# Optimization experiments

Hardware: AMD Instinct MI355X
Metric: run time of the kernel (lower is better)

Reference implementation:

```python
import jax, jax.numpy as jnp
import numpy as np

VOXEL_SIZE = 0.4
STRIDE = 2
NUM_BATCH = 4
PRE_MAXSIZE = 1024  # nms_premaxsize
NMS_THR = 0.1
NEG_INF = -1e9


def setup_inputs() -> dict:
    key = jax.random.key(0)
    ks = jax.random.split(key, 7)
    N, C = 200000, 256
    feat = jax.random.normal(ks[0], (N, C), dtype=jnp.float32)
    batch_idx = jax.random.randint(ks[1], (N,), 0, NUM_BATCH, dtype=jnp.int32)
    coor = jax.random.randint(ks[2], (N, 2), 0, 400, dtype=jnp.int32)
    W_cls = jax.random.normal(ks[3], (C, 2), dtype=jnp.float32) * 0.02
    b_cls = jnp.zeros((2,), dtype=jnp.float32)
    W_reg = jax.random.normal(ks[4], (C, 9), dtype=jnp.float32) * 0.02
    b_reg = jnp.zeros((9,), dtype=jnp.float32)
    return {"feat": feat, "batch_idx": batch_idx, "coor": coor,
            "W_cls": W_cls, "b_cls": b_cls, "W_reg": W_reg, "b_reg": b_reg}


def _bev_iou(bx):
    # bx: [K,7] (x,y,z,l,w,h,r); axis-aligned BEV IoU on (x,y,l,w)
    x, y, l, w = bx[:, 0], bx[:, 1], bx[:, 3], bx[:, 4]
    x1, x2 = x - l / 2, x + l / 2
    y1, y2 = y - w / 2, y + w / 2
    ix = jnp.maximum(jnp.minimum(x2[:, None], x2[None, :]) - jnp.maximum(x1[:, None], x1[None, :]), 0.0)
    iy = jnp.maximum(jnp.minimum(y2[:, None], y2[None, :]) - jnp.maximum(y1[:, None], y1[None, :]), 0.0)
    inter = ix * iy
    area = l * w
    union = area[:, None] + area[None, :] - inter
    return inter / jnp.maximum(union, 1e-6)


def _nms_keep(iou):
    # greedy NMS over score-descending rows; returns keep mask [K]
    K = iou.shape[0]
    idx = jnp.arange(K)

    def body(i, supp):
        keep_i = jnp.logical_not(supp[i])
        new = keep_i & (iou[i] > NMS_THR) & (idx > i)
        return supp | new

    supp = jax.lax.fori_loop(0, K, body, jnp.zeros((K,), dtype=bool))
    return jnp.logical_not(supp)


def reference(feat, batch_idx, coor, W_cls, b_cls, W_reg, b_reg):
    # ---- shared heads over all sparse voxels ----
    cls_logits = feat @ W_cls + b_cls            # [N, 1+1] (neg evidence, class)
    probs = jax.nn.softmax(cls_logits, axis=-1)
    cls_prob = probs[:, 1:]                      # [N, n_cls]
    conf = jnp.max(cls_prob, axis=-1)            # [N]
    label = jnp.argmax(cls_prob, axis=-1)        # [N]

    reg = feat @ W_reg + b_reg                   # [N, 9] -> ctr(3) dim(3) dir(2) scr(1)
    ctr, dim, drn, scr = reg[:, :3], reg[:, 3:6], reg[:, 6:8], reg[:, 8]
    scr = jax.nn.sigmoid(scr)                    # sigmoid_keys=['scr']

    # indices2metric: voxel indices -> metric centers
    centers = coor.astype(jnp.float32) * (VOXEL_SIZE * STRIDE)  # [N, 2]

    xy = centers + ctr[:, :2]
    z = ctr[:, 2]
    lwh = jnp.exp(jnp.clip(dim, -6.0, 6.0))
    angle = jnp.arctan2(drn[:, 0], drn[:, 1])
    boxes = jnp.concatenate([xy, z[:, None], lwh, angle[:, None]], axis=-1)  # [N, 7]
    score = conf * scr                           # [N]

    def per_sample(b):
        s = jnp.where(batch_idx == b, score, NEG_INF)
        vals, idx = jax.lax.top_k(s, PRE_MAXSIZE)          # score-sorted (desc)
        bx = boxes[idx]                                     # [K, 7]
        lb = label[idx]                                     # [K]
        valid = vals > NEG_INF / 2
        iou = _bev_iou(bx)
        keep = _nms_keep(iou) & valid
        out = jnp.concatenate([bx, vals[:, None]], axis=-1) * keep[:, None]  # [K, 8]
        return out, lb, keep

    out, lb, keep = jax.vmap(per_sample)(jnp.arange(NUM_BATCH))
    return out, lb, keep
```

## Files before the change

kernel.cpp:

```cpp
#include <hip/hip_runtime.h>
#include <math.h>

#define NBATCH 4
#define PRE 1024
#define CAND 4096
#define NHIST 65536

__device__ __forceinline__ unsigned long long allow_mask(int i, int l) {
    int base = l << 6;
    if (i < base) return ~0ull;
    int sh = i - base + 1;
    if (sh >= 64) return 0ull;
    return (~0ull) << sh;
}

__global__ void k0_weights(const float* __restrict__ Wcls, const float* __restrict__ bcls,
                           const float* __restrict__ Wreg, const float* __restrict__ breg,
                           double* __restrict__ Wd, double* __restrict__ biasd) {
    int j = blockIdx.x;
    int c = threadIdx.x;
    float w = (j < 2) ? Wcls[c * 2 + j] : Wreg[c * 9 + (j - 2)];
    Wd[j * 256 + c] = (double)w;
    if (c == 0) biasd[j] = (double)((j < 2) ? bcls[j] : breg[j - 2]);
}

__global__ __launch_bounds__(256) void k1_points(
    const float4* __restrict__ feat4, const int* __restrict__ batch_idx,
    const int* __restrict__ coor, const double* __restrict__ Wd,
    const double* __restrict__ biasd, float* __restrict__ pointData,
    unsigned long long* __restrict__ keys, unsigned int* __restrict__ hist, int N) {
    __shared__ float sfeat[256 * 33];
    int tid = threadIdx.x;
    int p0 = blockIdx.x * 256;

    double acc[11];
#pragma unroll
    for (int j = 0; j < 11; ++j) acc[j] = 0.0;

    for (int ch = 0; ch < 8; ++ch) {
        int c0 = ch * 32;
        __syncthreads();
#pragma unroll
        for (int it = 0; it < 8; ++it) {
            int u = it * 256 + tid;
            int p = u >> 3, q = u & 7;
            int gp = p0 + p;
            float4 v = make_float4(0.f, 0.f, 0.f, 0.f);
            if (gp < N) v = feat4[gp * 64 + (c0 >> 2) + q];
            int base = p * 33 + q * 4;
            sfeat[base + 0] = v.x; sfeat[base + 1] = v.y;
            sfeat[base + 2] = v.z; sfeat[base + 3] = v.w;
        }
        __syncthreads();
        const double* wb = Wd + c0;
#pragma unroll 4
        for (int k = 0; k < 32; ++k) {
            double fv = (double)sfeat[tid * 33 + k];
#pragma unroll
            for (int j = 0; j < 11; ++j) acc[j] = fma(fv, wb[j * 256 + k], acc[j]);
        }
    }

    int p = p0 + tid;
    if (p >= N) return;

    double l0 = acc[0] + biasd[0], l1 = acc[1] + biasd[1];
    double conf = 1.0 / (1.0 + exp(-(l1 - l0)));
    double scr  = 1.0 / (1.0 + exp(-(acc[10] + biasd[10])));
    double score = conf * scr;
    float s32 = (float)score;

    double c0d = acc[2] + biasd[2], c1d = acc[3] + biasd[3], c2d = acc[4] + biasd[4];
    double d0 = acc[5] + biasd[5], d1 = acc[6] + biasd[6], d2 = acc[7] + biasd[7];
    double r0 = acc[8] + biasd[8], r1 = acc[9] + biasd[9];

    float cx = (float)coor[2 * p] * 0.8f;
    float cy = (float)coor[2 * p + 1] * 0.8f;
    float bx = (float)((double)cx + c0d);
    float by = (float)((double)cy + c1d);
    float bz = (float)c2d;
    float bl = (float)exp(fmin(fmax(d0, -6.0), 6.0));
    float bw = (float)exp(fmin(fmax(d1, -6.0), 6.0));
    float bh = (float)exp(fmin(fmax(d2, -6.0), 6.0));
    float ba = (float)atan2(r0, r1);

    float* pd = pointData + (size_t)p * 8;
    pd[0] = bx; pd[1] = by; pd[2] = bz; pd[3] = bl;
    pd[4] = bw; pd[5] = bh; pd[6] = ba; pd[7] = s32;
    keys[p] = (unsigned long long)__double_as_longlong(score);

    int b = batch_idx[p];
    unsigned int bucket = __float_as_uint(s32) >> 16;
    atomicAdd(&hist[b * NHIST + bucket], 1u);
}

__global__ __launch_bounds__(256) void k2_thresh(const unsigned int* __restrict__ hist,
                                                 unsigned int* __restrict__ Tarr) {
    int b = blockIdx.x, tid = threadIdx.x;
    __shared__ unsigned int csum[256];
    __shared__ unsigned int chunkv[256];
    __shared__ int stc;
    __shared__ unsigned int scum;
    const unsigned int* h = hist + b * NHIST;
    unsigned int s = 0;
    for (int m = 0; m < 256; ++m) s += h[tid * 256 + m];
    csum[tid] = s;
    __syncthreads();
    if (tid == 0) {
        unsigned int cum = 0; int tc = -1;
        for (int t = 255; t >= 0; --t) {
            if (cum + csum[t] >= 1024u) { tc = t; break; }
            cum += csum[t];
        }
        stc = tc; scum = cum;
    }
    __syncthreads();
    int tc = stc;
    if (tc < 0) { if (tid == 0) Tarr[b] = 0u; return; }
    chunkv[tid] = h[tc * 256 + tid];
    __syncthreads();
    if (tid == 0) {
        unsigned int cum = scum, T = (unsigned int)(tc * 256);
        for (int m = 255; m >= 0; --m) {
            unsigned int c = chunkv[m];
            if (cum + c >= 1024u) { T = (unsigned int)(tc * 256 + m); break; }
            cum += c;
        }
        Tarr[b] = T;
    }
}

__global__ void k3_compact(const int* __restrict__ batch_idx, const float* __restrict__ pointData,
                           const unsigned long long* __restrict__ keys,
                           const unsigned int* __restrict__ Tarr, unsigned int* __restrict__ candCount,
                           unsigned int* __restrict__ candIdx, unsigned long long* __restrict__ candKey,
                           int N) {
    int p = blockIdx.x * 256 + threadIdx.x;
    if (p >= N) return;
    int b = batch_idx[p];
    float s32 = pointData[(size_t)p * 8 + 7];
    unsigned int bucket = __float_as_uint(s32) >> 16;
    if (bucket >= Tarr[b]) {
        unsigned int pos = atomicAdd(&candCount[b], 1u);
        if (pos < CAND) {
            candIdx[b * CAND + pos] = (unsigned int)p;
            candKey[b * CAND + pos] = keys[p];
        }
    }
}

__global__ __launch_bounds__(1024) void k4_sort(const unsigned int* __restrict__ candCount,
                                                const unsigned int* __restrict__ candIdx,
                                                const unsigned long long* __restrict__ candKey,
                                                const float* __restrict__ pointData,
                                                float* __restrict__ topBox,
                                                unsigned int* __restrict__ validArr) {
    int b = blockIdx.x, tid = threadIdx.x;
    __shared__ unsigned long long ka[CAND];
    __shared__ unsigned int id[CAND];
    unsigned int cnt = candCount[b];
    if (cnt > CAND) cnt = CAND;
    for (int t = tid; t < CAND; t += 1024) {
        if ((unsigned int)t < cnt) {
            ka[t] = ~candKey[b * CAND + t];
            id[t] = candIdx[b * CAND + t];
        } else {
            ka[t] = ~0ull;
            id[t] = 0xFFFFFFFFu;
        }
    }
    __syncthreads();
    for (int k = 2; k <= CAND; k <<= 1) {
        for (int j = k >> 1; j > 0; j >>= 1) {
            for (int t = tid; t < CAND; t += 1024) {
                int l = t ^ j;
                if (l > t) {
                    bool up = ((t & k) == 0);
                    unsigned long long kt = ka[t], kl = ka[l];
                    unsigned int it_ = id[t], il = id[l];
                    bool gt = (kt > kl) || (kt == kl && it_ > il);
                    if (gt == up) { ka[t] = kl; ka[l] = kt; id[t] = il; id[l] = it_; }
                }
            }
            __syncthreads();
        }
    }
    unsigned int gi = id[tid];
    bool valid = (gi != 0xFFFFFFFFu) && ((unsigned int)tid < cnt);
    float v[8];
#pragma unroll
    for (int k = 0; k < 8; ++k) v[k] = 0.f;
    if (valid) {
        const float* pd = pointData + (size_t)gi * 8;
#pragma unroll
        for (int k = 0; k < 8; ++k) v[k] = pd[k];
    }
    float* tb = topBox + (size_t)(b * PRE + tid) * 8;
#pragma unroll
    for (int k = 0; k < 8; ++k) tb[k] = v[k];
    validArr[b * PRE + tid] = valid ? 1u : 0u;
}

__global__ __launch_bounds__(256) void k5_iou(const float* __restrict__ topBox,
                                              unsigned long long* __restrict__ M) {
    int wid = blockIdx.x * 4 + (threadIdx.x >> 6);
    int lane = threadIdx.x & 63;
    int b = wid >> 14;
    int rem = wid & 16383;
    int i = rem >> 4;
    int wj = rem & 15;
    const float* bi = topBox + (size_t)(b * PRE + i) * 8;
    int j = wj * 64 + lane;
    const float* bj = topBox + (size_t)(b * PRE + j) * 8;
    float xi = bi[0], yi = bi[1], li = bi[3], wi_ = bi[4];
    float xj = bj[0], yj = bj[1], lj = bj[3], wj_ = bj[4];
    float x1i = xi - li * 0.5f, x2i = xi + li * 0.5f;
    float y1i = yi - wi_ * 0.5f, y2i = yi + wi_ * 0.5f;
    float x1j = xj - lj * 0.5f, x2j = xj + lj * 0.5f;
    float y1j = yj - wj_ * 0.5f, y2j = yj + wj_ * 0.5f;
    float ix = fmaxf(fminf(x2i, x2j) - fmaxf(x1i, x1j), 0.0f);
    float iy = fmaxf(fminf(y2i, y2j) - fmaxf(y1i, y1j), 0.0f);
    float inter = ix * iy;
    float ai = li * wi_, aj = lj * wj_;
    float uni = ai + aj - inter;
    float iou = inter / fmaxf(uni, 1e-6f);
    unsigned long long m = __ballot(iou > 0.1f);
    if (lane == 0) M[(size_t)(b * PRE + i) * 16 + wj] = m;
}

__global__ __launch_bounds__(256) void k6_nms(const unsigned long long* __restrict__ M,
                                              const unsigned int* __restrict__ validArr,
                                              const float* __restrict__ topBox,
                                              float* __restrict__ out0,
                                              float* __restrict__ keepOut) {
    int b = blockIdx.x, tid = threadIdx.x;
    __shared__ unsigned int flag[PRE];
    __shared__ unsigned long long suppSh[16];
    for (int r = tid; r < PRE; r += 256) {
        const unsigned long long* row = M + (size_t)(b * PRE + r) * 16;
        unsigned long long o = 0ull;
#pragma unroll
        for (int l = 0; l < 16; ++l) o |= row[l] & allow_mask(r, l);
        flag[r] = (o != 0ull) ? 1u : 0u;
    }
    __syncthreads();
    if (tid < 64) {
        int lane = tid;
        unsigned long long supp = 0ull;
        for (int g = 0; g < 16; ++g) {
            unsigned long long act = __ballot(flag[g * 64 + lane] != 0u);
            while (act) {
                int bit = __builtin_ctzll(act);
                act &= act - 1ull;
                int i = g * 64 + bit;
                unsigned long long w = __shfl(supp, i >> 6);
                bool keep_i = ((w >> (i & 63)) & 1ull) == 0ull;
                if (keep_i && lane < 16) {
                    supp |= M[(size_t)(b * PRE + i) * 16 + lane] & allow_mask(i, lane);
                }
            }
        }
        if (lane < 16) suppSh[lane] = supp;
    }
    __syncthreads();
    for (int r = tid; r < PRE; r += 256) {
        bool keep = (((suppSh[r >> 6] >> (r & 63)) & 1ull) == 0ull) && (validArr[b * PRE + r] != 0u);
        float kf = keep ? 1.0f : 0.0f;
        const float* tb = topBox + (size_t)(b * PRE + r) * 8;
        float* o = out0 + (size_t)(b * PRE + r) * 8;
#pragma unroll
        for (int k = 0; k < 8; ++k) o[k] = tb[k] * kf;
        keepOut[b * PRE + r] = kf;
    }
}

extern "C" void kernel_launch(void* const* d_in, const int* in_sizes, int n_in,
                              void* d_out, int out_size, void* d_ws, size_t ws_size,
                              hipStream_t stream) {
    int N = in_sizes[0] / 256;
    const float* feat = (const float*)d_in[0];
    const int* batch_idx = (const int*)d_in[1];
    const int* coor = (const int*)d_in[2];
    const float* Wcls = (const float*)d_in[3];
    const float* bcls = (const float*)d_in[4];
    const float* Wreg = (const float*)d_in[5];
    const float* breg = (const float*)d_in[6];

    char* ws = (char*)d_ws;
    size_t off = 0;
    auto take = [&](size_t bytes) -> char* {
        char* r = ws + off;
        off += (bytes + 255) & ~(size_t)255;
        return r;
    };
    float* pointData = (float*)take((size_t)N * 8 * 4);
    unsigned long long* keys = (unsigned long long*)take((size_t)N * 8);
    unsigned int* hist = (unsigned int*)take((size_t)NBATCH * NHIST * 4);
    unsigned int* Tarr = (unsigned int*)take(NBATCH * 4);
    unsigned int* candCount = (unsigned int*)take(NBATCH * 4);
    unsigned int* candIdx = (unsigned int*)take(NBATCH * CAND * 4);
    unsigned long long* candKey = (unsigned long long*)take(NBATCH * CAND * 8);
    float* topBox = (float*)take(NBATCH * PRE * 8 * 4);
    unsigned int* validArr = (unsigned int*)take(NBATCH * PRE * 4);
    unsigned long long* M = (unsigned long long*)take((size_t)NBATCH * PRE * 16 * 8);
    double* Wd = (double*)take(11 * 256 * 8);
    double* biasd = (double*)take(11 * 8);

    float* out0 = (float*)d_out;
    float* keepOut = out0 + NBATCH * PRE * 8 + NBATCH * PRE;

    hipMemsetAsync(d_out, 0, (size_t)out_size * 4, stream);
    hipMemsetAsync(hist, 0, (size_t)NBATCH * NHIST * 4, stream);
    hipMemsetAsync(candCount, 0, NBATCH * 4, stream);

    int pb = (N + 255) / 256;
    k0_weights<<<dim3(11), dim3(256), 0, stream>>>(Wcls, bcls, Wreg, breg, Wd, biasd);
    k1_points<<<dim3(pb), dim3(256), 0, stream>>>((const float4*)feat, batch_idx, coor,
                                                  Wd, biasd, pointData, keys, hist, N);
    k2_thresh<<<dim3(NBATCH), dim3(256), 0, stream>>>(hist, Tarr);
    k3_compact<<<dim3(pb), dim3(256), 0, stream>>>(batch_idx, pointData, keys, Tarr,
                                                   candCount, candIdx, candKey, N);
    k4_sort<<<dim3(NBATCH), dim3(1024), 0, stream>>>(candCount, candIdx, candKey,
                                                     pointData, topBox, validArr);
    k5_iou<<<dim3(NBATCH * PRE * 16 / 4), dim3(256), 0, stream>>>(topBox, M);
    k6_nms<<<dim3(NBATCH), dim3(256), 0, stream>>>(M, validArr, topBox, out0, keepOut);
}
```

Before: 506.2 us.

## Split head GEMV into fp64 score and fp32 box paths, shrink sort and NMS work

The point kernel now keeps only the class logits and score channel in double precision and computes the eight box-regression channels in fp32. It splits each point's 256 channels across four threads and reduces the partial sums through shared memory. The bitonic sort uses 2048 elements when the candidate count allows it, IoU warps skip tiles below the diagonal, and NMS caches the nonzero suppression rows in LDS so the serial loop avoids global reads. The fp32 box path can change rounding relative to the double path, and the 64-point blocks add a shared-memory reduction step.

```diff
diff --git a/kernel.cpp b/kernel.cpp
--- a/kernel.cpp
+++ b/kernel.cpp
@@ -5,6 +5,7 @@
 #define PRE 1024
 #define CAND 4096
 #define NHIST 65536
+#define MAXSLOT 384
 
 __device__ __forceinline__ unsigned long long allow_mask(int i, int l) {
     int base = l << 6;
@@ -16,82 +17,114 @@
 
 __global__ void k0_weights(const float* __restrict__ Wcls, const float* __restrict__ bcls,
                            const float* __restrict__ Wreg, const float* __restrict__ breg,
-                           double* __restrict__ Wd, double* __restrict__ biasd) {
+                           double* __restrict__ Wd3, float* __restrict__ Wf8,
+                           double* __restrict__ biasD, float* __restrict__ biasF) {
     int j = blockIdx.x;
     int c = threadIdx.x;
-    float w = (j < 2) ? Wcls[c * 2 + j] : Wreg[c * 9 + (j - 2)];
-    Wd[j * 256 + c] = (double)w;
-    if (c == 0) biasd[j] = (double)((j < 2) ? bcls[j] : breg[j - 2]);
+    if (j < 2) {
+        Wd3[j * 256 + c] = (double)Wcls[c * 2 + j];
+        if (c == 0) biasD[j] = (double)bcls[j];
+    } else if (j == 10) {
+        Wd3[2 * 256 + c] = (double)Wreg[c * 9 + 8];
+        if (c == 0) biasD[2] = (double)breg[8];
+    } else {
+        int r = j - 2;
+        Wf8[r * 256 + c] = Wreg[c * 9 + r];
+        if (c == 0) biasF[r] = breg[r];
+    }
 }
 
 __global__ __launch_bounds__(256) void k1_points(
     const float4* __restrict__ feat4, const int* __restrict__ batch_idx,
-    const int* __restrict__ coor, const double* __restrict__ Wd,
-    const double* __restrict__ biasd, float* __restrict__ pointData,
+    const int* __restrict__ coor, const double* __restrict__ Wd3,
+    const float* __restrict__ Wf8, const double* __restrict__ biasD,
+    const float* __restrict__ biasF, float* __restrict__ pointData,
     unsigned long long* __restrict__ keys, unsigned int* __restrict__ hist, int N) {
-    __shared__ float sfeat[256 * 33];
+    __shared__ float4 smem4[64 * 68 / 4];
+    float* sfeat = (float*)smem4;
     int tid = threadIdx.x;
-    int p0 = blockIdx.x * 256;
-
-    double acc[11];
-#pragma unroll
-    for (int j = 0; j < 11; ++j) acc[j] = 0.0;
-
-    for (int ch = 0; ch < 8; ++ch) {
-        int c0 = ch * 32;
+    int q = tid >> 6;
+    int p = tid & 63;
+    int p0 = blockIdx.x * 64;
+
+    double accD0 = 0.0, accD1 = 0.0, accD2 = 0.0;
+    float accF[8];
+#pragma unroll
+    for (int j = 0; j < 8; ++j) accF[j] = 0.f;
+
+    for (int c = 0; c < 4; ++c) {
         __syncthreads();
 #pragma unroll
-        for (int it = 0; it < 8; ++it) {
+        for (int it = 0; it < 4; ++it) {
             int u = it * 256 + tid;
-            int p = u >> 3, q = u & 7;
-            int gp = p0 + p;
+            int pl = u >> 4, f4 = u & 15;
+            int gp = p0 + pl;
             float4 v = make_float4(0.f, 0.f, 0.f, 0.f);
-            if (gp < N) v = feat4[gp * 64 + (c0 >> 2) + q];
-            int base = p * 33 + q * 4;
-            sfeat[base + 0] = v.x; sfeat[base + 1] = v.y;
-            sfeat[base + 2] = v.z; sfeat[base + 3] = v.w;
+            if (gp < N) v = feat4[(size_t)gp * 64 + c * 16 + f4];
+            *(float4*)(sfeat + pl * 68 + f4 * 4) = v;
         }
         __syncthreads();
-        const double* wb = Wd + c0;
-#pragma unroll 4
-        for (int k = 0; k < 32; ++k) {
-            double fv = (double)sfeat[tid * 33 + k];
-#pragma unroll
-            for (int j = 0; j < 11; ++j) acc[j] = fma(fv, wb[j * 256 + k], acc[j]);
-        }
-    }
-
-    int p = p0 + tid;
-    if (p >= N) return;
-
-    double l0 = acc[0] + biasd[0], l1 = acc[1] + biasd[1];
-    double conf = 1.0 / (1.0 + exp(-(l1 - l0)));
-    double scr  = 1.0 / (1.0 + exp(-(acc[10] + biasd[10])));
-    double score = conf * scr;
-    float s32 = (float)score;
-
-    double c0d = acc[2] + biasd[2], c1d = acc[3] + biasd[3], c2d = acc[4] + biasd[4];
-    double d0 = acc[5] + biasd[5], d1 = acc[6] + biasd[6], d2 = acc[7] + biasd[7];
-    double r0 = acc[8] + biasd[8], r1 = acc[9] + biasd[9];
-
-    float cx = (float)coor[2 * p] * 0.8f;
-    float cy = (float)coor[2 * p + 1] * 0.8f;
-    float bx = (float)((double)cx + c0d);
-    float by = (float)((double)cy + c1d);
-    float bz = (float)c2d;
-    float bl = (float)exp(fmin(fmax(d0, -6.0), 6.0));
-    float bw = (float)exp(fmin(fmax(d1, -6.0), 6.0));
-    float bh = (float)exp(fmin(fmax(d2, -6.0), 6.0));
-    float ba = (float)atan2(r0, r1);
-
-    float* pd = pointData + (size_t)p * 8;
-    pd[0] = bx; pd[1] = by; pd[2] = bz; pd[3] = bl;
-    pd[4] = bw; pd[5] = bh; pd[6] = ba; pd[7] = s32;
-    keys[p] = (unsigned long long)__double_as_longlong(score);
-
-    int b = batch_idx[p];
-    unsigned int bucket = __float_as_uint(s32) >> 16;
-    atomicAdd(&hist[b * NHIST + bucket], 1u);
+        int chb = c * 64 + q * 16;
+        const double* w0 = Wd3 + chb;
+        const float* wf = Wf8 + chb;
+#pragma unroll
+        for (int k4 = 0; k4 < 4; ++k4) {
+            float4 v = *(const float4*)(sfeat + p * 68 + q * 16 + k4 * 4);
+            float vv[4] = {v.x, v.y, v.z, v.w};
+#pragma unroll
+            for (int m = 0; m < 4; ++m) {
+                int k = k4 * 4 + m;
+                double fd = (double)vv[m];
+                accD0 = fma(fd, w0[k], accD0);
+                accD1 = fma(fd, w0[256 + k], accD1);
+                accD2 = fma(fd, w0[512 + k], accD2);
+#pragma unroll
+                for (int j = 0; j < 8; ++j) accF[j] = fmaf(vv[m], wf[j * 256 + k], accF[j]);
+            }
+        }
+    }
+    __syncthreads();
+    double* pD = (double*)smem4;
+    float* pF = (float*)smem4 + 1536;
+    pD[tid * 3 + 0] = accD0; pD[tid * 3 + 1] = accD1; pD[tid * 3 + 2] = accD2;
+#pragma unroll
+    for (int j = 0; j < 8; ++j) pF[tid * 8 + j] = accF[j];
+    __syncthreads();
+    if (tid < 64) {
+        int gp = p0 + tid;
+        if (gp < N) {
+            double d0 = biasD[0], d1 = biasD[1], d2 = biasD[2];
+            float f[8];
+#pragma unroll
+            for (int j = 0; j < 8; ++j) f[j] = biasF[j];
+#pragma unroll
+            for (int qq = 0; qq < 4; ++qq) {
+                int base = qq * 64 + tid;
+                d0 += pD[base * 3 + 0]; d1 += pD[base * 3 + 1]; d2 += pD[base * 3 + 2];
+#pragma unroll
+                for (int j = 0; j < 8; ++j) f[j] += pF[base * 8 + j];
+            }
+            double conf = 1.0 / (1.0 + exp(-(d1 - d0)));
+            double scr = 1.0 / (1.0 + exp(-d2));
+            double score = conf * scr;
+            float s32 = (float)score;
+
+            float cx = (float)coor[2 * gp] * 0.8f;
+            float cy = (float)coor[2 * gp + 1] * 0.8f;
+            float bx = cx + f[0], by = cy + f[1], bz = f[2];
+            float bl = expf(fminf(fmaxf(f[3], -6.f), 6.f));
+            float bw = expf(fminf(fmaxf(f[4], -6.f), 6.f));
+            float bh = expf(fminf(fmaxf(f[5], -6.f), 6.f));
+            float ba = atan2f(f[6], f[7]);
+
+            float4* pd = (float4*)(pointData + (size_t)gp * 8);
+            pd[0] = make_float4(bx, by, bz, bl);
+            pd[1] = make_float4(bw, bh, ba, s32);
+            keys[gp] = (unsigned long long)__double_as_longlong(score);
+            int b = batch_idx[gp];
+            atomicAdd(&hist[b * NHIST + (__float_as_uint(s32) >> 16)], 1u);
+        }
+    }
 }
 
 __global__ __launch_bounds__(256) void k2_thresh(const unsigned int* __restrict__ hist,
@@ -160,7 +193,8 @@
     __shared__ unsigned int id[CAND];
     unsigned int cnt = candCount[b];
     if (cnt > CAND) cnt = CAND;
-    for (int t = tid; t < CAND; t += 1024) {
+    int n = (cnt <= 2048u) ? 2048 : 4096;
+    for (int t = tid; t < n; t += 1024) {
         if ((unsigned int)t < cnt) {
             ka[t] = ~candKey[b * CAND + t];
             id[t] = candIdx[b * CAND + t];
@@ -170,9 +204,9 @@
         }
     }
     __syncthreads();
-    for (int k = 2; k <= CAND; k <<= 1) {
+    for (int k = 2; k <= n; k <<= 1) {
         for (int j = k >> 1; j > 0; j >>= 1) {
-            for (int t = tid; t < CAND; t += 1024) {
+            for (int t = tid; t < n; t += 1024) {
                 int l = t ^ j;
                 if (l > t) {
                     bool up = ((t & k) == 0);
@@ -209,6 +243,7 @@
     int rem = wid & 16383;
     int i = rem >> 4;
     int wj = rem & 15;
+    if (wj < (i >> 6)) return;
     const float* bi = topBox + (size_t)(b * PRE + i) * 8;
     int j = wj * 64 + lane;
     const float* bj = topBox + (size_t)(b * PRE + j) * 8;
@@ -233,30 +268,48 @@
                                               const float* __restrict__ topBox,
                                               float* __restrict__ out0,
                                               float* __restrict__ keepOut) {
+    __shared__ unsigned long long Mc[MAXSLOT * 16];
+    __shared__ unsigned int slotIdx[PRE];
+    __shared__ unsigned int cntSh;
+    __shared__ unsigned long long suppSh[16];
     int b = blockIdx.x, tid = threadIdx.x;
-    __shared__ unsigned int flag[PRE];
-    __shared__ unsigned long long suppSh[16];
+    if (tid == 0) cntSh = 0;
+    __syncthreads();
     for (int r = tid; r < PRE; r += 256) {
         const unsigned long long* row = M + (size_t)(b * PRE + r) * 16;
+        unsigned long long w[16];
         unsigned long long o = 0ull;
 #pragma unroll
-        for (int l = 0; l < 16; ++l) o |= row[l] & allow_mask(r, l);
-        flag[r] = (o != 0ull) ? 1u : 0u;
+        for (int l = 0; l < 16; ++l) { w[l] = row[l] & allow_mask(r, l); o |= w[l]; }
+        unsigned int s = 0xFFFFFFFFu;
+        if (o != 0ull) {
+            unsigned int slot = atomicAdd(&cntSh, 1u);
+            if (slot < MAXSLOT) {
+                s = slot;
+#pragma unroll
+                for (int l = 0; l < 16; ++l) Mc[slot * 16 + l] = w[l];
+            } else s = 0xFFFFFFFEu;
+        }
+        slotIdx[r] = s;
     }
     __syncthreads();
     if (tid < 64) {
         int lane = tid;
         unsigned long long supp = 0ull;
         for (int g = 0; g < 16; ++g) {
-            unsigned long long act = __ballot(flag[g * 64 + lane] != 0u);
+            unsigned long long act = __ballot(slotIdx[g * 64 + lane] != 0xFFFFFFFFu);
             while (act) {
                 int bit = __builtin_ctzll(act);
                 act &= act - 1ull;
                 int i = g * 64 + bit;
-                unsigned long long w = __shfl(supp, i >> 6);
-                bool keep_i = ((w >> (i & 63)) & 1ull) == 0ull;
+                unsigned long long wsup = __shfl(supp, g);
+                bool keep_i = ((wsup >> (i & 63)) & 1ull) == 0ull;
                 if (keep_i && lane < 16) {
-                    supp |= M[(size_t)(b * PRE + i) * 16 + lane] & allow_mask(i, lane);
+                    unsigned int s = slotIdx[i];
+                    unsigned long long add = (s < MAXSLOT)
+                        ? Mc[s * 16 + lane]
+                        : (M[(size_t)(b * PRE + i) * 16 + lane] & allow_mask(i, lane));
+                    supp |= add;
                 }
             }
         }
@@ -303,8 +356,10 @@
     float* topBox = (float*)take(NBATCH * PRE * 8 * 4);
     unsigned int* validArr = (unsigned int*)take(NBATCH * PRE * 4);
     unsigned long long* M = (unsigned long long*)take((size_t)NBATCH * PRE * 16 * 8);
-    double* Wd = (double*)take(11 * 256 * 8);
-    double* biasd = (double*)take(11 * 8);
+    double* Wd3 = (double*)take(3 * 256 * 8);
+    float* Wf8 = (float*)take(8 * 256 * 4);
+    double* biasD = (double*)take(3 * 8);
+    float* biasF = (float*)take(8 * 4);
 
     float* out0 = (float*)d_out;
     float* keepOut = out0 + NBATCH * PRE * 8 + NBATCH * PRE;
@@ -313,13 +368,15 @@
     hipMemsetAsync(hist, 0, (size_t)NBATCH * NHIST * 4, stream);
     hipMemsetAsync(candCount, 0, NBATCH * 4, stream);
 
-    int pb = (N + 255) / 256;
-    k0_weights<<<dim3(11), dim3(256), 0, stream>>>(Wcls, bcls, Wreg, breg, Wd, biasd);
-    k1_points<<<dim3(pb), dim3(256), 0, stream>>>((const float4*)feat, batch_idx, coor,
-                                                  Wd, biasd, pointData, keys, hist, N);
+    int pb64 = (N + 63) / 64;
+    int pb256 = (N + 255) / 256;
+    k0_weights<<<dim3(11), dim3(256), 0, stream>>>(Wcls, bcls, Wreg, breg, Wd3, Wf8, biasD, biasF);
+    k1_points<<<dim3(pb64), dim3(256), 0, stream>>>((const float4*)feat, batch_idx, coor,
+                                                    Wd3, Wf8, biasD, biasF,
+                                                    pointData, keys, hist, N);
     k2_thresh<<<dim3(NBATCH), dim3(256), 0, stream>>>(hist, Tarr);
-    k3_compact<<<dim3(pb), dim3(256), 0, stream>>>(batch_idx, pointData, keys, Tarr,
-                                                   candCount, candIdx, candKey, N);
+    k3_compact<<<dim3(pb256), dim3(256), 0, stream>>>(batch_idx, pointData, keys, Tarr,
+                                                      candCount, candIdx, candKey, N);
     k4_sort<<<dim3(NBATCH), dim3(1024), 0, stream>>>(candCount, candIdx, candKey,
                                                      pointData, topBox, validArr);
     k5_iou<<<dim3(NBATCH * PRE * 16 / 4), dim3(256), 0, stream>>>(topBox, M);
```

Measured after the change: 488.3 us. 1.04x faster.
